# Performance work log

Hardware: AMD Instinct MI355X
Metric: run time of the kernel (lower is better)

The kernel has to match this reference:

```python
import jax, jax.numpy as jnp
import numpy as np

B, T, V, D = 64, 128, 50000, 1024  # batch, num_steps, vocab_size, size


def setup_inputs() -> dict:
    key = jax.random.key(0)
    ks = jax.random.split(key, 5)
    inputs = jax.random.randint(ks[0], (B, T), 0, V, dtype=jnp.int32)
    input_lengths = jax.random.randint(ks[1], (B,), 0, T, dtype=jnp.int32)
    emb = jax.random.normal(ks[2], (V, D), dtype=jnp.float32) * 0.1  # ~truncated_normal(-0.1,0.1)
    # BasicLSTMCell weights: [input_dim + hidden, 4*hidden]
    W1 = jax.random.normal(ks[3], (2 * D, 4 * D), dtype=jnp.float32) / np.sqrt(2 * D)
    b1 = jnp.zeros((4 * D,), dtype=jnp.float32)
    W2 = jax.random.normal(ks[4], (2 * D, 4 * D), dtype=jnp.float32) / np.sqrt(2 * D)
    b2 = jnp.zeros((4 * D,), dtype=jnp.float32)
    return {"inputs": inputs, "input_lengths": input_lengths,
            "emb": emb, "W1": W1, "b1": b1, "W2": W2, "b2": b2}


def _lstm_cell(c, h, x, W, b):
    # BasicLSTMCell with forget_bias=0.0
    gates = jnp.concatenate([x, h], axis=-1) @ W + b  # [B, 4D]
    i, j, f, o = jnp.split(gates, 4, axis=-1)
    c_new = c * jax.nn.sigmoid(f) + jax.nn.sigmoid(i) * jnp.tanh(j)
    h_new = jnp.tanh(c_new) * jax.nn.sigmoid(o)
    return c_new, h_new


def reference(inputs, input_lengths, emb, W1, b1, W2, b2):
    # embedding_lookup on transposed inputs -> time-major [T, B, D]
    x_seq = jnp.transpose(emb[inputs], (1, 0, 2))
    # sequence_length semantics of tf rnn.rnn: past length, output is zero
    # and state is carried through unchanged.
    mask = (jnp.arange(T)[:, None] < input_lengths[None, :]).astype(emb.dtype)  # [T, B]

    def step(carry, xm):
        c1, h1, c2, h2 = carry
        x_t, m_t = xm
        m = m_t[:, None]  # [B, 1]
        c1n, h1n = _lstm_cell(c1, h1, x_t, W1, b1)
        c2n, h2n = _lstm_cell(c2, h2, h1n, W2, b2)
        c1 = m * c1n + (1.0 - m) * c1
        h1 = m * h1n + (1.0 - m) * h1
        c2 = m * c2n + (1.0 - m) * c2
        h2 = m * h2n + (1.0 - m) * h2
        out_t = h2n * m  # zero output past sequence end
        return (c1, h1, c2, h2), out_t

    zeros = jnp.zeros((B, D), dtype=emb.dtype)
    init = (zeros, zeros, zeros, zeros)
    _, outs = jax.lax.scan(step, init, (x_seq, mask))  # outs: [T, B, D]
    return outs.sum(axis=0)  # reduce_sum over time -> [B, D]
```

## Files before the change

kernel.cpp:

```cpp
#include <hip/hip_runtime.h>

#define B_ 64
#define T_ 128
#define D_ 1024
#define K2_ 2048
#define G_ 4096
#define SLOTW 65664

typedef __attribute__((ext_vector_type(8))) short bf16x8;
typedef __attribute__((ext_vector_type(4))) float f32x4;
typedef unsigned short u16;
typedef unsigned long long u64;

__device__ __forceinline__ u16 f2bf(float f) {
  unsigned int u = __float_as_uint(f);
  u += 0x7FFF + ((u >> 16) & 1);
  return (u16)(u >> 16);
}

__device__ __forceinline__ float fast_sigmoid(float x) {
  return 1.f / (1.f + __expf(-x));
}
__device__ __forceinline__ float fast_tanh(float x) {
  float e = __expf(-2.f * fabsf(x));
  float t = (1.f - e) / (1.f + e);
  return copysignf(t, x);
}

__device__ __forceinline__ void store4_wt(u16* addr, unsigned v) {
  asm volatile("global_store_dword %0, %1, off sc0 sc1"
               :: "v"((void*)addr), "v"(v) : "memory");
}

__device__ __forceinline__ void store_pair_wt(u16* base, size_t soff, u16 v, int tid) {
  unsigned other = __shfl_xor((unsigned)v, 1);
  if (!(tid & 1))
    store4_wt(base + soff, (unsigned)v | (other << 16));
}

__global__ __launch_bounds__(256) void transpose_w(const float* __restrict__ W,
                                                   u16* __restrict__ Wt) {
  __shared__ u16 tile[64][65];
  int bn = blockIdx.x & 63;
  int bk = blockIdx.x >> 6;
  int n0 = bn * 64, k0 = bk * 64;
  for (int i = threadIdx.x; i < 4096; i += 256) {
    int r = i >> 6, c = i & 63;
    tile[c][r] = f2bf(W[(size_t)(k0 + r) * G_ + n0 + c]);
  }
  __syncthreads();
  for (int i = threadIdx.x; i < 4096; i += 256) {
    int r = i >> 6, c = i & 63;
    Wt[(size_t)(n0 + r) * K2_ + k0 + c] = tile[r][c];
  }
}

__global__ __launch_bounds__(256) void gather_x(const int* __restrict__ inputs,
                                                const float* __restrict__ emb,
                                                u16* __restrict__ xg) {
  int idx = blockIdx.x * 256 + threadIdx.x;
  int d4 = idx & 255;
  int tb = idx >> 8;
  int t = tb >> 6, b = tb & 63;
  int tok = inputs[b * T_ + t];
  float4 v = ((const float4*)(emb + (size_t)tok * D_))[d4];
  u64 pk = (u64)f2bf(v.x)
         | ((u64)f2bf(v.y) << 16)
         | ((u64)f2bf(v.z) << 32)
         | ((u64)f2bf(v.w) << 48);
  *(u64*)(xg + (size_t)tb * D_ + d4 * 4) = pk;
}

__global__ void zero_buf(uint4* p, int n) {
  int i = blockIdx.x * blockDim.x + threadIdx.x;
  if (i < n) p[i] = make_uint4(0u, 0u, 0u, 0u);
}

#define GRPBASE(L, rg, i) (16 + (((L) * 2 + (rg)) * 129 + (i)) * 9)

__device__ __forceinline__ void poll_root(const int* bar, int base) {
  while (__hip_atomic_load(bar + (size_t)(base + 8) * 32,
                           __ATOMIC_RELAXED, __HIP_MEMORY_SCOPE_AGENT) < 8)
    __builtin_amdgcn_s_sleep(1);
}

__global__ __launch_bounds__(512, 2) void lstm_persist(
    const u16* wt1, const u16* wt2,
    const u16* __restrict__ xg,
    u16* h1buf, u16* h1n, u16* h2buf,
    const u16* __restrict__ zbuf,
    const float* __restrict__ b1, const float* __restrict__ b2,
    const int* __restrict__ lens, float* __restrict__ out,
    int* bar) {
  __shared__ __attribute__((aligned(16))) float part[8][64][36];
  __shared__ __attribute__((aligned(16))) float gsum[64][36];
  const int blk = blockIdx.x;
  const int L = blk >> 7;
  const int lb = blk & 127;
  const int rg = lb & 1;
  const int cg = lb >> 1;
  const int tid = threadIdx.x;
  const int lane = tid & 63;
  const int wv = tid >> 6;
  const int dc = lane & 15;
  const int kq = lane >> 4;

  const u16* wt = L ? wt2 : wt1;
  const float* bias = L ? b2 : b1;

  bf16x8 wreg[4][8];
  {
    const u16* wb = wt + (size_t)(cg * 16 + dc) * K2_ + wv * 256 + kq * 8;
    #pragma unroll
    for (int g = 0; g < 4; ++g)
      #pragma unroll
      for (int ks = 0; ks < 8; ++ks)
        wreg[g][ks] = *(const bf16x8*)(wb + (size_t)g * D_ * K2_ + ks * 32);
  }
  #pragma unroll
  for (int g = 0; g < 4; ++g)
    #pragma unroll
    for (int ks = 0; ks < 8; ++ks)
      asm volatile("" : "+v"(wreg[g][ks]));

  const int crow = tid >> 4;
  const int cdc = tid & 15;
  const int grow = rg * 32 + crow;
  const int dcol = cg * 16 + cdc;
  const int len_r = lens[grow];
  float bias_g[4];
  #pragma unroll
  for (int g = 0; g < 4; ++g) bias_g[g] = bias[g * D_ + dcol];
  float creg = 0.f, hreg = 0.f, outreg = 0.f;

  const int r0 = rg * 32 + (lane & 15);
  const int koff = (wv & 3) * 256 + kq * 8;

  __syncthreads();
  if (tid == 0) {
    int a = __hip_atomic_fetch_add(bar + (size_t)(blk & 7) * 32, 1,
                                   __ATOMIC_RELAXED, __HIP_MEMORY_SCOPE_AGENT);
    if (a == 31) {
      int r = __hip_atomic_fetch_add(bar + 8 * 32, 1,
                                     __ATOMIC_RELAXED, __HIP_MEMORY_SCOPE_AGENT);
      if (r == 7)
        __hip_atomic_store(bar + 9 * 32, 1,
                           __ATOMIC_RELAXED, __HIP_MEMORY_SCOPE_AGENT);
    }
    while (!__hip_atomic_load(bar + 9 * 32,
                              __ATOMIC_RELAXED, __HIP_MEMORY_SCOPE_AGENT))
      __builtin_amdgcn_s_sleep(1);
  }
  __syncthreads();
  __builtin_amdgcn_fence(__ATOMIC_ACQUIRE, "agent");

  for (int i = 0; i <= 128; ++i) {
    const bool active = L ? (i >= 1) : (i < 128);
    const int t = L ? i - 1 : i;
    if (active) {
      if (tid == 0 && i >= 1) {
        if (L == 0) {
          poll_root(bar, GRPBASE(0, rg, i - 1));
        } else {
          poll_root(bar, GRPBASE(0, rg, i - 1));
          if (i >= 2) poll_root(bar, GRPBASE(1, rg, i - 1));
        }
      }
      __syncthreads();

      const u16* xsrc; const u16* hsrc;
      u16* w_h1n = nullptr; u16* w_h1b = nullptr; u16* w_h2b = nullptr;
      if (L == 0) {
        xsrc = xg + (size_t)t * (B_ * D_);
        hsrc = (i == 0) ? zbuf : h1buf + (size_t)(i - 1) * SLOTW;
        w_h1n = h1n + (size_t)i * SLOTW;
        w_h1b = h1buf + (size_t)i * SLOTW;
      } else {
        xsrc = h1n + (size_t)(i - 1) * SLOTW;
        hsrc = (i <= 1) ? zbuf : h2buf + (size_t)(i - 2) * SLOTW;
        w_h2b = h2buf + (size_t)(i - 1) * SLOTW;
      }
      const u16* src = (wv < 4) ? xsrc : hsrc;
      const u16* a0p = src + (size_t)r0 * D_ + koff;

      f32x4 acc[2][4];
      #pragma unroll
      for (int rt = 0; rt < 2; ++rt)
        #pragma unroll
        for (int g = 0; g < 4; ++g)
          acc[rt][g] = (f32x4){0.f, 0.f, 0.f, 0.f};

      #pragma unroll
      for (int ks = 0; ks < 8; ++ks) {
        bf16x8 a0 = *(const bf16x8*)(a0p + ks * 32);
        bf16x8 a1 = *(const bf16x8*)(a0p + 16 * D_ + ks * 32);
        #pragma unroll
        for (int g = 0; g < 4; ++g) {
          acc[0][g] = __builtin_amdgcn_mfma_f32_16x16x32_bf16(a0, wreg[g][ks], acc[0][g], 0, 0, 0);
          acc[1][g] = __builtin_amdgcn_mfma_f32_16x16x32_bf16(a1, wreg[g][ks], acc[1][g], 0, 0, 0);
        }
      }

      #pragma unroll
      for (int rt = 0; rt < 2; ++rt)
        #pragma unroll
        for (int g = 0; g < 4; ++g)
          *(f32x4*)&part[wv][g * 16 + dc][rt * 16 + kq * 4] = acc[rt][g];
      __syncthreads();

      {
        const int rcol = tid >> 3;
        const int rrow = (tid & 7) * 4;
        f32x4 s = *(const f32x4*)&part[0][rcol][rrow];
        #pragma unroll
        for (int w = 1; w < 8; ++w) s += *(const f32x4*)&part[w][rcol][rrow];
        *(f32x4*)&gsum[rcol][rrow] = s;
      }
      __syncthreads();

      {
        float gi = gsum[cdc][crow] + bias_g[0];
        float gj = gsum[16 + cdc][crow] + bias_g[1];
        float gf = gsum[32 + cdc][crow] + bias_g[2];
        float go = gsum[48 + cdc][crow] + bias_g[3];
        float is = fast_sigmoid(gi);
        float fs = fast_sigmoid(gf);
        float os = fast_sigmoid(go);
        float jt = fast_tanh(gj);
        float c_new = creg * fs + is * jt;
        float h_new = fast_tanh(c_new) * os;
        bool m = t < len_r;
        if (m) { creg = c_new; hreg = h_new; }
        size_t soff = (size_t)grow * D_ + dcol;
        if (L == 0) {
          store_pair_wt(w_h1n, soff, f2bf(h_new), tid);
          store_pair_wt(w_h1b, soff, f2bf(hreg), tid);
        } else {
          store_pair_wt(w_h2b, soff, f2bf(hreg), tid);
          if (m) outreg += h_new;
        }
      }

      asm volatile("s_waitcnt vmcnt(0)" ::: "memory");
      __syncthreads();
      if (tid == 0 && !(L == 1 && i == 128)) {
        int base = GRPBASE(L, rg, i);
        int a = __hip_atomic_fetch_add(bar + (size_t)(base + (cg & 7)) * 32, 1,
                                       __ATOMIC_RELAXED, __HIP_MEMORY_SCOPE_AGENT);
        if (a == 7)
          __hip_atomic_fetch_add(bar + (size_t)(base + 8) * 32, 1,
                                 __ATOMIC_RELAXED, __HIP_MEMORY_SCOPE_AGENT);
      }
    }
  }
  if (L == 1) out[(size_t)grow * D_ + dcol] = outreg;
}

extern "C" void kernel_launch(void* const* d_in, const int* in_sizes, int n_in,
                              void* d_out, int out_size, void* d_ws, size_t ws_size,
                              hipStream_t stream) {
  const int* inputs  = (const int*)d_in[0];
  const int* lengths = (const int*)d_in[1];
  const float* emb   = (const float*)d_in[2];
  const float* W1    = (const float*)d_in[3];
  const float* b1    = (const float*)d_in[4];
  const float* W2    = (const float*)d_in[5];
  const float* b2    = (const float*)d_in[6];
  float* out = (float*)d_out;

  char* p = (char*)d_ws;
  u16* h1buf = (u16*)p; p += (size_t)T_ * SLOTW * 2;
  u16* h1n   = (u16*)p; p += (size_t)T_ * SLOTW * 2;
  u16* h2buf = (u16*)p; p += (size_t)T_ * SLOTW * 2;
  u16* xg    = (u16*)p; p += (size_t)T_ * B_ * D_ * 2;
  u16* zbuf  = (u16*)p; p += (size_t)B_ * D_ * 2;
  int* bar   = (int*)p; p += (size_t)4672 * 128;
  u16* wt1 = h1buf;
  u16* wt2 = h1n;

  hipLaunchKernelGGL(transpose_w, dim3(2048), dim3(256), 0, stream, W1, wt1);
  hipLaunchKernelGGL(transpose_w, dim3(2048), dim3(256), 0, stream, W2, wt2);
  hipLaunchKernelGGL(gather_x, dim3(8192), dim3(256), 0, stream, inputs, emb, xg);
  hipLaunchKernelGGL(zero_buf, dim3(178), dim3(256), 0, stream, (uint4*)zbuf, 45568);

  hipLaunchKernelGGL(lstm_persist, dim3(256), dim3(512), 0, stream,
                     wt1, wt2, xg, h1buf, h1n, h2buf, zbuf, b1, b2, lengths, out,
                     bar);
}
```

Before: 936.5 us.

## Use per-wave fine-grained step barriers and fuse gate reduction into the cell update

Replaces the two-level counter tree with one counter per group of 8 column groups, and drops the block-wide poll by thread 0. Each wave now polls only the two counters covering the 256-column K slice it reads from x or h, so waves can start their MFMAs as soon as their own inputs are ready. This cuts the root-counter hop and a __syncthreads from the per-step critical path. The cross-wave partial sums are also reduced directly inside the gate computation, which removes the gsum shared buffer and another block barrier at the cost of some redundant LDS reads. The counter workspace and its zeroing are shrunk to match.

```diff
diff --git a/kernel.cpp b/kernel.cpp
--- a/kernel.cpp
+++ b/kernel.cpp
@@ -76,13 +76,7 @@
   if (i < n) p[i] = make_uint4(0u, 0u, 0u, 0u);
 }
 
-#define GRPBASE(L, rg, i) (16 + (((L) * 2 + (rg)) * 129 + (i)) * 9)
-
-__device__ __forceinline__ void poll_root(const int* bar, int base) {
-  while (__hip_atomic_load(bar + (size_t)(base + 8) * 32,
-                           __ATOMIC_RELAXED, __HIP_MEMORY_SCOPE_AGENT) < 8)
-    __builtin_amdgcn_s_sleep(1);
-}
+#define GRPBASE(L, rg, i) (16 + (((L) * 2 + (rg)) * 129 + (i)) * 8)
 
 __global__ __launch_bounds__(512, 2) void lstm_persist(
     const u16* wt1, const u16* wt2,
@@ -93,7 +87,6 @@
     const int* __restrict__ lens, float* __restrict__ out,
     int* bar) {
   __shared__ __attribute__((aligned(16))) float part[8][64][36];
-  __shared__ __attribute__((aligned(16))) float gsum[64][36];
   const int blk = blockIdx.x;
   const int L = blk >> 7;
   const int lb = blk & 127;
@@ -158,15 +151,18 @@
     const bool active = L ? (i >= 1) : (i < 128);
     const int t = L ? i - 1 : i;
     if (active) {
-      if (tid == 0 && i >= 1) {
-        if (L == 0) {
-          poll_root(bar, GRPBASE(0, rg, i - 1));
-        } else {
-          poll_root(bar, GRPBASE(0, rg, i - 1));
-          if (i >= 2) poll_root(bar, GRPBASE(1, rg, i - 1));
-        }
-      }
-      __syncthreads();
+      if (i >= 1) {
+        int grp = -1;
+        if (L == 0) { if (wv >= 4) grp = 0; }
+        else        { grp = (wv < 4) ? 0 : (i >= 2 ? 1 : -1); }
+        if (grp >= 0 && lane < 2) {
+          const int* lp = bar + (size_t)(GRPBASE(grp, rg, i - 1)
+                                         + 2 * (wv & 3) + lane) * 32;
+          while (__hip_atomic_load(lp, __ATOMIC_RELAXED,
+                                   __HIP_MEMORY_SCOPE_AGENT) < 8)
+            __builtin_amdgcn_s_sleep(1);
+        }
+      }
 
       const u16* xsrc; const u16* hsrc;
       u16* w_h1n = nullptr; u16* w_h1b = nullptr; u16* w_h2b = nullptr;
@@ -209,24 +205,18 @@
       __syncthreads();
 
       {
-        const int rcol = tid >> 3;
-        const int rrow = (tid & 7) * 4;
-        f32x4 s = *(const f32x4*)&part[0][rcol][rrow];
-        #pragma unroll
-        for (int w = 1; w < 8; ++w) s += *(const f32x4*)&part[w][rcol][rrow];
-        *(f32x4*)&gsum[rcol][rrow] = s;
-      }
-      __syncthreads();
-
-      {
-        float gi = gsum[cdc][crow] + bias_g[0];
-        float gj = gsum[16 + cdc][crow] + bias_g[1];
-        float gf = gsum[32 + cdc][crow] + bias_g[2];
-        float go = gsum[48 + cdc][crow] + bias_g[3];
-        float is = fast_sigmoid(gi);
-        float fs = fast_sigmoid(gf);
-        float os = fast_sigmoid(go);
-        float jt = fast_tanh(gj);
+        float gacc[4];
+        #pragma unroll
+        for (int g = 0; g < 4; ++g) {
+          float s = part[0][g * 16 + cdc][crow];
+          #pragma unroll
+          for (int w = 1; w < 8; ++w) s += part[w][g * 16 + cdc][crow];
+          gacc[g] = s + bias_g[g];
+        }
+        float is = fast_sigmoid(gacc[0]);
+        float jt = fast_tanh(gacc[1]);
+        float fs = fast_sigmoid(gacc[2]);
+        float os = fast_sigmoid(gacc[3]);
         float c_new = creg * fs + is * jt;
         float h_new = fast_tanh(c_new) * os;
         bool m = t < len_r;
@@ -243,14 +233,9 @@
 
       asm volatile("s_waitcnt vmcnt(0)" ::: "memory");
       __syncthreads();
-      if (tid == 0 && !(L == 1 && i == 128)) {
-        int base = GRPBASE(L, rg, i);
-        int a = __hip_atomic_fetch_add(bar + (size_t)(base + (cg & 7)) * 32, 1,
-                                       __ATOMIC_RELAXED, __HIP_MEMORY_SCOPE_AGENT);
-        if (a == 7)
-          __hip_atomic_fetch_add(bar + (size_t)(base + 8) * 32, 1,
-                                 __ATOMIC_RELAXED, __HIP_MEMORY_SCOPE_AGENT);
-      }
+      if (tid == 0 && !(L == 1 && i == 128))
+        __hip_atomic_fetch_add(bar + (size_t)(GRPBASE(L, rg, i) + (cg >> 3)) * 32, 1,
+                               __ATOMIC_RELAXED, __HIP_MEMORY_SCOPE_AGENT);
     }
   }
   if (L == 1) out[(size_t)grow * D_ + dcol] = outreg;
@@ -274,14 +259,14 @@
   u16* h2buf = (u16*)p; p += (size_t)T_ * SLOTW * 2;
   u16* xg    = (u16*)p; p += (size_t)T_ * B_ * D_ * 2;
   u16* zbuf  = (u16*)p; p += (size_t)B_ * D_ * 2;
-  int* bar   = (int*)p; p += (size_t)4672 * 128;
+  int* bar   = (int*)p; p += (size_t)4144 * 128;
   u16* wt1 = h1buf;
   u16* wt2 = h1n;
 
   hipLaunchKernelGGL(transpose_w, dim3(2048), dim3(256), 0, stream, W1, wt1);
   hipLaunchKernelGGL(transpose_w, dim3(2048), dim3(256), 0, stream, W2, wt2);
   hipLaunchKernelGGL(gather_x, dim3(8192), dim3(256), 0, stream, inputs, emb, xg);
-  hipLaunchKernelGGL(zero_buf, dim3(178), dim3(256), 0, stream, (uint4*)zbuf, 45568);
+  hipLaunchKernelGGL(zero_buf, dim3(162), dim3(256), 0, stream, (uint4*)zbuf, 41344);
 
   hipLaunchKernelGGL(lstm_persist, dim3(256), dim3(512), 0, stream,
                      wt1, wt2, xg, h1buf, h1n, h2buf, zbuf, b1, b2, lengths, out,
```

Result: faster. 889.7 us (median of 2 runs) (-5.0%).
